# Kernel tuning notes

Measured on AMD Instinct MI355X. Metric: run time of the kernel, lower is better.

Reference implementation:

```python
import jax, jax.numpy as jnp
import numpy as np

B, C, H, W = 16, 512, 96, 48
SE_C = C // 16  # se bottleneck = 32
BN_EPS = 1e-5


def setup_inputs() -> dict:
    key = jax.random.key(0)
    ks = jax.random.split(key, 16)
    s = 0.02
    return {
        "x": jax.random.normal(ks[0], (B, C, H, W), jnp.float32),
        # SE gate: C -> SE_C -> C (1x1 convs stored as dense matrices)
        "se_w1": jax.random.normal(ks[1], (SE_C, C), jnp.float32) * s,
        "se_b1": jnp.zeros((SE_C,), jnp.float32),
        "se_w2": jax.random.normal(ks[2], (C, SE_C), jnp.float32) * s,
        "se_b2": jnp.zeros((C,), jnp.float32),
        # g / theta / phi: 1x1 convs C -> 1 (weight is a C-vector, scalar bias)
        "g_w": jax.random.normal(ks[3], (C,), jnp.float32) * s,
        "g_b": jnp.zeros((), jnp.float32),
        "theta_w": jax.random.normal(ks[4], (C,), jnp.float32) * s,
        "theta_b": jnp.zeros((), jnp.float32),
        "phi_w": jax.random.normal(ks[5], (C,), jnp.float32) * s,
        "phi_b": jnp.zeros((), jnp.float32),
        # W: 1x1 conv 1 -> C, followed by BatchNorm2d(C) (inference stats).
        # NOTE: torch inits BN gamma/beta to 0 (output would be exactly x);
        # we use random gamma/beta so the whole graph contributes to output/grads.
        "W_w": jax.random.normal(ks[6], (C,), jnp.float32) * s,
        "W_b": jnp.zeros((C,), jnp.float32),
        "bn_gamma": jax.random.normal(ks[7], (C,), jnp.float32) * 0.1 + 1.0,
        "bn_beta": jax.random.normal(ks[8], (C,), jnp.float32) * 0.1,
        "bn_mean": jax.random.normal(ks[9], (C,), jnp.float32) * 0.1,
        "bn_var": jax.random.uniform(ks[10], (C,), jnp.float32, 0.5, 1.5),
    }


def reference(x, se_w1, se_b1, se_w2, se_b2, g_w, g_b, theta_w, theta_b,
              phi_w, phi_b, W_w, W_b, bn_gamma, bn_beta, bn_mean, bn_var):
    b, c, h, w = x.shape
    n = h * w
    # SE channel gate on global-avg-pooled features
    xp = x.mean(axis=(2, 3))                                  # (b, c)
    hid = jax.nn.relu(xp @ se_w1.T + se_b1)                   # (b, se_c)
    gate = jax.nn.sigmoid(hid @ se_w2.T + se_b2)              # (b, c)
    xc = gate[:, :, None, None] * x                           # (b, c, h, w)
    # 1x1 C->1 projections, flattened over spatial positions
    g_x = jnp.einsum('bchw,c->bhw', xc, g_w).reshape(b, n) + g_b       # (b, n)
    th = jnp.einsum('bchw,c->bhw', xc, theta_w).reshape(b, n) + theta_b
    ph = jnp.einsum('bchw,c->bhw', xc, phi_w).reshape(b, n) + phi_b
    # f = theta phi^T / N; y = f g. inter_channels==1 => rank-1, contract phi.g first
    s = jnp.sum(ph * g_x, axis=-1, keepdims=True) / n          # (b, 1)
    y = (th * s).reshape(b, 1, h, w)                           # (b, 1, h, w)
    # W: 1x1 conv 1->C then BatchNorm2d (inference form)
    wy = y * W_w[None, :, None, None] + W_b[None, :, None, None]
    inv = bn_gamma / jnp.sqrt(bn_var + BN_EPS)
    wy = (wy - bn_mean[None, :, None, None]) * inv[None, :, None, None] \
         + bn_beta[None, :, None, None]
    return wy + x
```

## Files before the change

### kernel.cpp

```cpp
#include <hip/hip_runtime.h>
#include <math.h>

#define BB   16
#define CCH  512
#define HWN  4608
#define HW4  1152
#define HW2  2304
#define NSE  32
#define BN_EPS 1e-5f

#define NCH  8
#define CPC  64

typedef float f32x4 __attribute__((ext_vector_type(4)));

__global__ __launch_bounds__(256) void k_mean(const float* __restrict__ x,
                                              float* __restrict__ xp) {
    int wave = threadIdx.x >> 6;
    int lane = threadIdx.x & 63;
    int row = blockIdx.x * 4 + wave;
    const float4* xr = (const float4*)x + (size_t)row * HW4;
    float s = 0.f;
    #pragma unroll
    for (int k = 0; k < 18; ++k) {
        float4 v = xr[lane + k * 64];
        s += v.x + v.y + v.z + v.w;
    }
    #pragma unroll
    for (int off = 32; off > 0; off >>= 1)
        s += __shfl_down(s, off);
    if (lane == 0) xp[row] = s * (1.0f / (float)HWN);
}

__global__ __launch_bounds__(512) void k_gate(
    const float* __restrict__ xp,
    const float* __restrict__ se_w1, const float* __restrict__ se_b1,
    const float* __restrict__ se_w2, const float* __restrict__ se_b2,
    const float* __restrict__ g_w, const float* __restrict__ theta_w,
    const float* __restrict__ phi_w,
    float* __restrict__ tw, float* __restrict__ pw, float* __restrict__ gw) {
    __shared__ float xs[CCH];
    __shared__ float hs[NSE];
    int b = blockIdx.x, t = threadIdx.x;
    int wave = t >> 6, lane = t & 63;
    xs[t] = xp[b * CCH + t];
    __syncthreads();
    #pragma unroll
    for (int i = 0; i < 4; ++i) {
        int h = wave * 4 + i;
        const float* wr = se_w1 + h * CCH;
        float a = 0.f;
        #pragma unroll
        for (int k = 0; k < 8; ++k)
            a += wr[lane + 64 * k] * xs[lane + 64 * k];
        #pragma unroll
        for (int off = 32; off > 0; off >>= 1)
            a += __shfl_down(a, off);
        if (lane == 0) {
            a += se_b1[h];
            hs[h] = a > 0.f ? a : 0.f;
        }
    }
    __syncthreads();
    float a = se_b2[t];
    const float* wr = se_w2 + t * NSE;
    #pragma unroll
    for (int j = 0; j < NSE; ++j) a += wr[j] * hs[j];
    float gate = 1.f / (1.f + expf(-a));
    int idx = b * CCH + t;
    tw[idx] = gate * theta_w[t];
    pw[idx] = gate * phi_w[t];
    gw[idx] = gate * g_w[t];
}

__global__ __launch_bounds__(256) void k_proj(
    const float* __restrict__ x,
    const float* __restrict__ tw, const float* __restrict__ pw,
    const float* __restrict__ gw,
    float* __restrict__ th_part, float* __restrict__ ph_part,
    float* __restrict__ gx_part) {
    __shared__ float tws[CPC], pws[CPC], gws[CPC];
    int t = threadIdx.x;
    int b = blockIdx.z;
    int ch = blockIdx.y;
    int c0 = ch * CPC;
    int p2 = blockIdx.x * 256 + t;
    if (t < CPC) {
        int wi = b * CCH + c0 + t;
        tws[t] = tw[wi]; pws[t] = pw[wi]; gws[t] = gw[wi];
    }
    __syncthreads();
    const float2* xr = (const float2*)x + (size_t)(b * CCH + c0) * HW2 + p2;
    float2 tha = {0.f, 0.f}, pha = {0.f, 0.f}, gxa = {0.f, 0.f};
    #pragma unroll 8
    for (int c = 0; c < CPC; ++c) {
        float2 v = xr[(size_t)c * HW2];
        float tc = tws[c], pc = pws[c], gc = gws[c];
        tha.x += tc * v.x; tha.y += tc * v.y;
        pha.x += pc * v.x; pha.y += pc * v.y;
        gxa.x += gc * v.x; gxa.y += gc * v.y;
    }
    size_t oi = (size_t)(ch * BB + b) * HW2 + p2;
    ((float2*)th_part)[oi] = tha;
    ((float2*)ph_part)[oi] = pha;
    ((float2*)gx_part)[oi] = gxa;
}

__global__ __launch_bounds__(256) void k_scale(
    const float* __restrict__ th_part, const float* __restrict__ ph_part,
    const float* __restrict__ gx_part,
    const float* __restrict__ theta_b, const float* __restrict__ phi_b,
    const float* __restrict__ g_b,
    float* __restrict__ ths) {
    __shared__ float red[256];
    int b = blockIdx.x, t = threadIdx.x;
    float pb = phi_b[0], gb = g_b[0];
    const float4* php = (const float4*)ph_part;
    const float4* gxp = (const float4*)gx_part;
    float acc = 0.f;
    for (int i = t; i < HW4; i += 256) {
        float4 ph = {pb, pb, pb, pb};
        float4 gx = {gb, gb, gb, gb};
        #pragma unroll
        for (int k = 0; k < NCH; ++k) {
            size_t oi = (size_t)(k * BB + b) * HW4 + i;
            float4 pv = php[oi];
            float4 gv = gxp[oi];
            ph.x += pv.x; ph.y += pv.y; ph.z += pv.z; ph.w += pv.w;
            gx.x += gv.x; gx.y += gv.y; gx.z += gv.z; gx.w += gv.w;
        }
        acc += ph.x * gx.x + ph.y * gx.y + ph.z * gx.z + ph.w * gx.w;
    }
    red[t] = acc;
    __syncthreads();
    for (int off = 128; off > 0; off >>= 1) {
        if (t < off) red[t] += red[t + off];
        __syncthreads();
    }
    float s = red[0] * (1.0f / (float)HWN);
    float tb = theta_b[0];
    const float4* thp = (const float4*)th_part;
    float4* out4 = (float4*)ths;
    for (int i = t; i < HW4; i += 256) {
        float4 th = {tb, tb, tb, tb};
        #pragma unroll
        for (int k = 0; k < NCH; ++k) {
            float4 tv = thp[(size_t)(k * BB + b) * HW4 + i];
            th.x += tv.x; th.y += tv.y; th.z += tv.z; th.w += tv.w;
        }
        float4 o;
        o.x = th.x * s; o.y = th.y * s; o.z = th.z * s; o.w = th.w * s;
        out4[(size_t)b * HW4 + i] = o;
    }
}

__global__ __launch_bounds__(256) void k_out(
    const float* __restrict__ x, const float* __restrict__ ths,
    const float* __restrict__ W_w, const float* __restrict__ W_b,
    const float* __restrict__ bn_gamma, const float* __restrict__ bn_beta,
    const float* __restrict__ bn_mean, const float* __restrict__ bn_var,
    float* __restrict__ out) {
    int wave = threadIdx.x >> 6;
    int lane = threadIdx.x & 63;
    int c = blockIdx.x * 4 + wave;
    int b = blockIdx.y;
    float inv = bn_gamma[c] * rsqrtf(bn_var[c] + BN_EPS);
    float A = W_w[c] * inv;
    float Dc = (W_b[c] - bn_mean[c]) * inv + bn_beta[c];
    const float4* xr = (const float4*)x + (size_t)(b * CCH + c) * HW4;
    const float4* tr = (const float4*)ths + (size_t)b * HW4;
    f32x4* orow = (f32x4*)out + (size_t)(b * CCH + c) * HW4;
    #pragma unroll
    for (int k = 0; k < 18; ++k) {
        int i = lane + k * 64;
        float4 xv = xr[i];
        float4 tv = tr[i];
        f32x4 o;
        o.x = xv.x + tv.x * A + Dc;
        o.y = xv.y + tv.y * A + Dc;
        o.z = xv.z + tv.z * A + Dc;
        o.w = xv.w + tv.w * A + Dc;
        __builtin_nontemporal_store(o, &orow[i]);
    }
}

extern "C" void kernel_launch(void* const* d_in, const int* in_sizes, int n_in,
                              void* d_out, int out_size, void* d_ws, size_t ws_size,
                              hipStream_t stream) {
    const float* x       = (const float*)d_in[0];
    const float* se_w1   = (const float*)d_in[1];
    const float* se_b1   = (const float*)d_in[2];
    const float* se_w2   = (const float*)d_in[3];
    const float* se_b2   = (const float*)d_in[4];
    const float* g_w     = (const float*)d_in[5];
    const float* g_b     = (const float*)d_in[6];
    const float* theta_w = (const float*)d_in[7];
    const float* theta_b = (const float*)d_in[8];
    const float* phi_w   = (const float*)d_in[9];
    const float* phi_b   = (const float*)d_in[10];
    const float* W_w     = (const float*)d_in[11];
    const float* W_b     = (const float*)d_in[12];
    const float* bn_g    = (const float*)d_in[13];
    const float* bn_b    = (const float*)d_in[14];
    const float* bn_m    = (const float*)d_in[15];
    const float* bn_v    = (const float*)d_in[16];
    float* out = (float*)d_out;

    float* ws      = (float*)d_ws;
    float* xp      = ws;
    float* tw      = ws + 8192;
    float* pw      = ws + 16384;
    float* gwv     = ws + 24576;
    float* th_part = ws + 32768;
    float* ph_part = ws + 32768 + 589824;
    float* gx_part = ws + 32768 + 2 * 589824;
    float* ths     = ws + 32768 + 3 * 589824;

    k_mean<<<BB * CCH / 4, 256, 0, stream>>>(x, xp);
    k_gate<<<BB, CCH, 0, stream>>>(xp, se_w1, se_b1, se_w2, se_b2,
                                   g_w, theta_w, phi_w, tw, pw, gwv);
    dim3 gc(9, NCH, BB);
    k_proj<<<gc, 256, 0, stream>>>(x, tw, pw, gwv, th_part, ph_part, gx_part);
    k_scale<<<BB, 256, 0, stream>>>(th_part, ph_part, gx_part,
                                    theta_b, phi_b, g_b, ths);
    dim3 gd(CCH / 4, BB);
    k_out<<<gd, 256, 0, stream>>>(x, ths, W_w, W_b, bn_g, bn_b, bn_m, bn_v, out);
}
```

Measured before the change: 338.4 us.

## Split per-batch scale reduction into parallel atomic reduce and apply kernels

Replaces the 16-block k_scale kernel with two grid-parallel kernels: one reduces phi·g partials per batch via wave shuffles and atomicAdd into an accumulator zeroed in k_gate, and one sums theta partials and applies the scale. The aim is to remove the low-parallelism serial loop over spatial positions that left most CUs idle. k_proj is also widened to float4 loads with 128-thread blocks. This adds an extra kernel launch, and atomic float accumulation makes the summation order nondeterministic.

```diff
diff --git a/kernel.cpp b/kernel.cpp
--- a/kernel.cpp
+++ b/kernel.cpp
@@ -38,11 +38,13 @@
     const float* __restrict__ se_w2, const float* __restrict__ se_b2,
     const float* __restrict__ g_w, const float* __restrict__ theta_w,
     const float* __restrict__ phi_w,
-    float* __restrict__ tw, float* __restrict__ pw, float* __restrict__ gw) {
+    float* __restrict__ tw, float* __restrict__ pw, float* __restrict__ gw,
+    float* __restrict__ sacc) {
     __shared__ float xs[CCH];
     __shared__ float hs[NSE];
     int b = blockIdx.x, t = threadIdx.x;
     int wave = t >> 6, lane = t & 63;
+    if (t == 0) sacc[b] = 0.f;
     xs[t] = xp[b * CCH + t];
     __syncthreads();
     #pragma unroll
@@ -73,7 +75,7 @@
     gw[idx] = gate * g_w[t];
 }
 
-__global__ __launch_bounds__(256) void k_proj(
+__global__ __launch_bounds__(128) void k_proj(
     const float* __restrict__ x,
     const float* __restrict__ tw, const float* __restrict__ pw,
     const float* __restrict__ gw,
@@ -84,74 +86,77 @@
     int b = blockIdx.z;
     int ch = blockIdx.y;
     int c0 = ch * CPC;
-    int p2 = blockIdx.x * 256 + t;
+    int p4 = blockIdx.x * 128 + t;
     if (t < CPC) {
         int wi = b * CCH + c0 + t;
         tws[t] = tw[wi]; pws[t] = pw[wi]; gws[t] = gw[wi];
     }
     __syncthreads();
-    const float2* xr = (const float2*)x + (size_t)(b * CCH + c0) * HW2 + p2;
-    float2 tha = {0.f, 0.f}, pha = {0.f, 0.f}, gxa = {0.f, 0.f};
+    const float4* xr = (const float4*)x + (size_t)(b * CCH + c0) * HW4 + p4;
+    float4 tha = {0.f, 0.f, 0.f, 0.f};
+    float4 pha = {0.f, 0.f, 0.f, 0.f};
+    float4 gxa = {0.f, 0.f, 0.f, 0.f};
     #pragma unroll 8
     for (int c = 0; c < CPC; ++c) {
-        float2 v = xr[(size_t)c * HW2];
+        float4 v = xr[(size_t)c * HW4];
         float tc = tws[c], pc = pws[c], gc = gws[c];
-        tha.x += tc * v.x; tha.y += tc * v.y;
-        pha.x += pc * v.x; pha.y += pc * v.y;
-        gxa.x += gc * v.x; gxa.y += gc * v.y;
-    }
-    size_t oi = (size_t)(ch * BB + b) * HW2 + p2;
-    ((float2*)th_part)[oi] = tha;
-    ((float2*)ph_part)[oi] = pha;
-    ((float2*)gx_part)[oi] = gxa;
-}
-
-__global__ __launch_bounds__(256) void k_scale(
-    const float* __restrict__ th_part, const float* __restrict__ ph_part,
-    const float* __restrict__ gx_part,
-    const float* __restrict__ theta_b, const float* __restrict__ phi_b,
-    const float* __restrict__ g_b,
-    float* __restrict__ ths) {
-    __shared__ float red[256];
-    int b = blockIdx.x, t = threadIdx.x;
+        tha.x += tc * v.x; tha.y += tc * v.y; tha.z += tc * v.z; tha.w += tc * v.w;
+        pha.x += pc * v.x; pha.y += pc * v.y; pha.z += pc * v.z; pha.w += pc * v.w;
+        gxa.x += gc * v.x; gxa.y += gc * v.y; gxa.z += gc * v.z; gxa.w += gc * v.w;
+    }
+    size_t oi = (size_t)(ch * BB + b) * HW4 + p4;
+    ((float4*)th_part)[oi] = tha;
+    ((float4*)ph_part)[oi] = pha;
+    ((float4*)gx_part)[oi] = gxa;
+}
+
+__global__ __launch_bounds__(128) void k_sred(
+    const float* __restrict__ ph_part, const float* __restrict__ gx_part,
+    const float* __restrict__ phi_b, const float* __restrict__ g_b,
+    float* __restrict__ sacc) {
+    int t = threadIdx.x;
+    int b = blockIdx.y;
+    int i = blockIdx.x * 128 + t;
     float pb = phi_b[0], gb = g_b[0];
     const float4* php = (const float4*)ph_part;
     const float4* gxp = (const float4*)gx_part;
-    float acc = 0.f;
-    for (int i = t; i < HW4; i += 256) {
-        float4 ph = {pb, pb, pb, pb};
-        float4 gx = {gb, gb, gb, gb};
-        #pragma unroll
-        for (int k = 0; k < NCH; ++k) {
-            size_t oi = (size_t)(k * BB + b) * HW4 + i;
-            float4 pv = php[oi];
-            float4 gv = gxp[oi];
-            ph.x += pv.x; ph.y += pv.y; ph.z += pv.z; ph.w += pv.w;
-            gx.x += gv.x; gx.y += gv.y; gx.z += gv.z; gx.w += gv.w;
-        }
-        acc += ph.x * gx.x + ph.y * gx.y + ph.z * gx.z + ph.w * gx.w;
-    }
-    red[t] = acc;
-    __syncthreads();
-    for (int off = 128; off > 0; off >>= 1) {
-        if (t < off) red[t] += red[t + off];
-        __syncthreads();
-    }
-    float s = red[0] * (1.0f / (float)HWN);
+    float4 ph = {pb, pb, pb, pb};
+    float4 gx = {gb, gb, gb, gb};
+    #pragma unroll
+    for (int k = 0; k < NCH; ++k) {
+        size_t oi = (size_t)(k * BB + b) * HW4 + i;
+        float4 pv = php[oi];
+        float4 gv = gxp[oi];
+        ph.x += pv.x; ph.y += pv.y; ph.z += pv.z; ph.w += pv.w;
+        gx.x += gv.x; gx.y += gv.y; gx.z += gv.z; gx.w += gv.w;
+    }
+    float acc = ph.x * gx.x + ph.y * gx.y + ph.z * gx.z + ph.w * gx.w;
+    #pragma unroll
+    for (int off = 32; off > 0; off >>= 1)
+        acc += __shfl_down(acc, off);
+    __shared__ float ws0;
+    if (t == 64) ws0 = acc;
+    __syncthreads();
+    if (t == 0) atomicAdd(&sacc[b], acc + ws0);
+}
+
+__global__ __launch_bounds__(128) void k_ths(
+    const float* __restrict__ th_part, const float* __restrict__ theta_b,
+    const float* __restrict__ sacc, float* __restrict__ ths) {
+    int t = threadIdx.x;
+    int b = blockIdx.y;
+    int i = blockIdx.x * 128 + t;
+    float s = sacc[b] * (1.0f / (float)HWN);
     float tb = theta_b[0];
     const float4* thp = (const float4*)th_part;
-    float4* out4 = (float4*)ths;
-    for (int i = t; i < HW4; i += 256) {
-        float4 th = {tb, tb, tb, tb};
-        #pragma unroll
-        for (int k = 0; k < NCH; ++k) {
-            float4 tv = thp[(size_t)(k * BB + b) * HW4 + i];
-            th.x += tv.x; th.y += tv.y; th.z += tv.z; th.w += tv.w;
-        }
-        float4 o;
-        o.x = th.x * s; o.y = th.y * s; o.z = th.z * s; o.w = th.w * s;
-        out4[(size_t)b * HW4 + i] = o;
-    }
+    float4 th = {tb, tb, tb, tb};
+    #pragma unroll
+    for (int k = 0; k < NCH; ++k) {
+        float4 tv = thp[(size_t)(k * BB + b) * HW4 + i];
+        th.x += tv.x; th.y += tv.y; th.z += tv.z; th.w += tv.w;
+    }
+    float4 o = {th.x * s, th.y * s, th.z * s, th.w * s};
+    ((float4*)ths)[(size_t)b * HW4 + i] = o;
 }
 
 __global__ __launch_bounds__(256) void k_out(
@@ -215,14 +220,16 @@
     float* ph_part = ws + 32768 + 589824;
     float* gx_part = ws + 32768 + 2 * 589824;
     float* ths     = ws + 32768 + 3 * 589824;
+    float* sacc    = ws + 32768 + 3 * 589824 + 73728;
 
     k_mean<<<BB * CCH / 4, 256, 0, stream>>>(x, xp);
     k_gate<<<BB, CCH, 0, stream>>>(xp, se_w1, se_b1, se_w2, se_b2,
-                                   g_w, theta_w, phi_w, tw, pw, gwv);
+                                   g_w, theta_w, phi_w, tw, pw, gwv, sacc);
     dim3 gc(9, NCH, BB);
-    k_proj<<<gc, 256, 0, stream>>>(x, tw, pw, gwv, th_part, ph_part, gx_part);
-    k_scale<<<BB, 256, 0, stream>>>(th_part, ph_part, gx_part,
-                                    theta_b, phi_b, g_b, ths);
+    k_proj<<<gc, 128, 0, stream>>>(x, tw, pw, gwv, th_part, ph_part, gx_part);
+    dim3 gs(9, BB);
+    k_sred<<<gs, 128, 0, stream>>>(ph_part, gx_part, phi_b, g_b, sacc);
+    k_ths<<<gs, 128, 0, stream>>>(th_part, theta_b, sacc, ths);
     dim3 gd(CCH / 4, BB);
     k_out<<<gd, 256, 0, stream>>>(x, ths, W_w, W_b, bn_g, bn_b, bn_m, bn_v, out);
 }
```

Result: no change. 339.9 us (+0.5%).
